# Kernel optimization log

Hardware: AMD Instinct MI355X
Metric: run time of the kernel (lower is better)

## Reference

```python
import jax, jax.numpy as jnp
import numpy as np

N_RAYS, MAX_S, N_VOX, EMB, HID, L_VIEW = 8192, 64, 100000, 32, 128, 4


def view_pe(d):
    # NeRF positional encoding of view dirs: [N,3] -> [N, 3 + 6*L_VIEW]
    freqs = 2.0 ** jnp.arange(L_VIEW, dtype=d.dtype)
    ang = (d[..., None] * freqs).reshape(*d.shape[:-1], -1)  # [N, 3*L]
    return jnp.concatenate([d, jnp.sin(ang), jnp.cos(ang)], -1)


def setup_inputs() -> dict:
    key = jax.random.key(0)
    ks = jax.random.split(key, 16)
    rays_d = jax.random.normal(ks[0], (N_RAYS, 3), dtype=jnp.float32)
    rays_d = rays_d / jnp.linalg.norm(rays_d, axis=-1, keepdims=True)
    pts = jax.random.uniform(ks[1], (N_RAYS, MAX_S, 3), dtype=jnp.float32)
    t_vals = jnp.sort(jax.random.uniform(ks[2], (N_RAYS, MAX_S), dtype=jnp.float32) * 4.0, axis=-1)
    dists = jnp.concatenate([t_vals[:, 1:] - t_vals[:, :-1], jnp.full((N_RAYS, 1), 0.05, jnp.float32)], -1)
    # ragged per-ray sample counts -> -1 padded p2v_idx (as produced by the voxel point sampler)
    counts = jax.random.randint(ks[3], (N_RAYS,), 1, MAX_S + 1)
    ray_hits = jax.random.bernoulli(ks[4], 0.9, (N_RAYS,))
    valid = (jnp.arange(MAX_S)[None, :] < counts[:, None]) & ray_hits[:, None]
    idx = jax.random.randint(ks[5], (N_RAYS, MAX_S), 0, N_VOX)
    p2v_idx = jnp.where(valid, idx, -1).astype(jnp.int32)

    def lin(k, i, o):
        return jax.random.normal(k, (i, o), dtype=jnp.float32) * np.float32(1.0 / np.sqrt(i))

    return dict(
        rays_d=rays_d, pts=pts, t_vals=t_vals, dists=dists,
        p2v_idx=p2v_idx, ray_hits=ray_hits,
        vox_emb=jax.random.normal(ks[6], (N_VOX, EMB), dtype=jnp.float32) * 0.1,
        Wpts=lin(ks[7], 3, EMB),
        W1=lin(ks[8], EMB, HID), b1=jnp.zeros((HID,), jnp.float32),
        W2=lin(ks[9], HID, HID), b2=jnp.zeros((HID,), jnp.float32),
        Wsig=lin(ks[10], HID, 1), bsig=jnp.zeros((1,), jnp.float32),
        Wfeat=lin(ks[11], HID, HID), bfeat=jnp.zeros((HID,), jnp.float32),
        Wc1=lin(ks[12], HID + 3 + 6 * L_VIEW, 64), bc1=jnp.zeros((64,), jnp.float32),
        Wc2=lin(ks[13], 64, 3), bc2=jnp.zeros((3,), jnp.float32),
    )


def reference(rays_d, pts, t_vals, dists, vox_emb, Wpts, W1, b1, W2, b2,
              Wsig, bsig, Wfeat, bfeat, Wc1, bc1, Wc2, bc2, p2v_idx, ray_hits):
    mask = p2v_idx >= 0                                   # [N,S] valid samples (mask_pts)
    idx = jnp.where(mask, p2v_idx, 0)
    # voxel_embedder: per-point voxel embedding gather + positional lift
    ve = vox_emb[idx] + pts @ Wpts                        # [N,S,EMB]
    h = jax.nn.relu(ve @ W1 + b1)
    h = jax.nn.relu(h @ W2 + b2)                          # [N,S,HID]
    sigma = (h @ Wsig + bsig)[..., 0]                     # [N,S]
    feat = h @ Wfeat + bfeat                              # [N,S,HID]
    vemb = view_pe(rays_d)                                # [N,27]
    vemb = jnp.broadcast_to(vemb[:, None, :], (feat.shape[0], feat.shape[1], vemb.shape[-1]))
    c = jax.nn.relu(jnp.concatenate([feat, vemb], -1) @ Wc1 + bc1)
    rgb_raw = c @ Wc2 + bc2                               # [N,S,3]
    # masked_scatter semantics: invalid slots are 0 before the min_color remap
    rgb = (jnp.where(mask[..., None], rgb_raw, 0.0) + 1.0) * 0.5   # min_color = -1
    free_energy = jnp.where(mask, jax.nn.relu(sigma) * dists, 0.0)  # [N,S]
    # volumetric_rendering(with_dist=True)
    shifted = jnp.concatenate([jnp.zeros_like(free_energy[:, :1]), free_energy[:, :-1]], -1)
    T = jnp.exp(-jnp.cumsum(shifted, -1))
    weights = (1.0 - jnp.exp(-free_energy)) * T           # [N,S]
    comp_rgb = jnp.einsum('ns,nsc->nc', weights, rgb)     # [N,3]
    acc = weights.sum(-1)                                 # [N]
    depth = (weights * t_vals).sum(-1)
    disp = 1.0 / jnp.maximum(1e-10, depth / jnp.maximum(acc, 1e-10))
    # fill_in for missed rays (white_bkgd=False -> fill with 0)
    comp_rgb = jnp.where(ray_hits[:, None], comp_rgb, 0.0)
    disp = jnp.where(ray_hits, disp, 0.0)
    acc = jnp.where(ray_hits, acc, 0.0)
    return comp_rgb, disp, acc
```

## Files before the change

### kernel.cpp

```cpp
#include <hip/hip_runtime.h>
#include <stdint.h>


#define NRAYS 8192
#define MAXS  64
#define EMB   32
#define HID   128
#define NPE   27
#define CH    64
#define NPTS  (NRAYS * MAXS)
#define RCAP  16384

#define WS_WCOMB  0
#define WS_WPE    (WS_WCOMB + HID*CH)
#define WS_BCOMB  (WS_WPE + 32*CH)
#define WS_CCINIT (WS_BCOMB + CH)
#define WS_COUNTS (WS_CCINIT + NRAYS*CH)
#define WS_OFFS   (WS_COUNTS + NRAYS)
#define WS_TOTAL  (WS_OFFS + NRAYS)
#define WS_RCNT   (WS_TOTAL + 1)
#define WS_LIST   (WS_TOTAL + 4)
#define WS_PTOUT  (WS_LIST + NPTS)
#define WS_FRAGS  (WS_PTOUT + 4*NPTS)
#define WS_RLIST  (WS_FRAGS + 56*2*64*4)
#define WS_PTSC   (WS_RLIST + RCAP)

typedef __attribute__((ext_vector_type(8))) short bf16x8;
typedef __attribute__((ext_vector_type(4))) float f32x4;
union FI { int i[4]; int4 v; bf16x8 f; };

#define MFMA16(a, b, c) __builtin_amdgcn_mfma_f32_16x16x32_bf16(a, b, c, 0, 0, 0)

__device__ __forceinline__ f32x4 mfma3(bf16x8 ah, bf16x8 al, bf16x8 bh, bf16x8 bl,
                                       f32x4 c) {
  c = MFMA16(al, bh, c);
  c = MFMA16(ah, bl, c);
  c = MFMA16(ah, bh, c);
  return c;
}

__device__ __forceinline__ void split8(const float* x, bf16x8& hi, bf16x8& lo) {
  FI H, L;
#pragma unroll
  for (int r = 0; r < 4; ++r) {
    unsigned u0 = __float_as_uint(x[2 * r]);
    unsigned u1 = __float_as_uint(x[2 * r + 1]);
    unsigned h0 = u0 & 0xffff0000u, h1 = u1 & 0xffff0000u;
    unsigned l0 = __float_as_uint(x[2 * r] - __uint_as_float(h0));
    unsigned l1 = __float_as_uint(x[2 * r + 1] - __uint_as_float(h1));
    H.i[r] = (int)((h0 >> 16) | (h1 & 0xffff0000u));
    L.i[r] = (int)((l0 >> 16) | (l1 & 0xffff0000u));
  }
  hi = H.f; lo = L.f;
}

__device__ __forceinline__ int packword(float v) {
  unsigned u = __float_as_uint(v);
  unsigned hb = u & 0xffff0000u;
  unsigned lb = __float_as_uint(v - __uint_as_float(hb));
  return (int)((u >> 16) | (lb & 0xffff0000u));
}

__device__ __forceinline__ void unpack8(const int* w, bf16x8& hi, bf16x8& lo) {
  FI H, L;
#pragma unroll
  for (int r = 0; r < 4; ++r) {
    unsigned w0 = (unsigned)w[2 * r], w1 = (unsigned)w[2 * r + 1];
    H.i[r] = (int)((w0 & 0xffffu) | (w1 << 16));
    L.i[r] = (int)((w0 >> 16) | (w1 & 0xffff0000u));
  }
  hi = H.f; lo = L.f;
}

__global__ __launch_bounds__(256) void prep_kernel(
    const float* __restrict__ Wfeat, const float* __restrict__ bfeat,
    const float* __restrict__ Wc1, const float* __restrict__ bc1,
    float* __restrict__ ws) {
  int idx = blockIdx.x * 256 + threadIdx.x;
  if (idx < HID * CH) {
    int m = idx >> 6, j = idx & 63;
    float s = 0.f;
    for (int f = 0; f < HID; ++f) s = fmaf(Wfeat[m * HID + f], Wc1[f * CH + j], s);
    ws[WS_WCOMB + idx] = s;
    return;
  }
  idx -= HID * CH;
  if (idx < 32 * CH) {
    int v = idx >> 6, j = idx & 63;
    ws[WS_WPE + idx] = (v < NPE) ? Wc1[(HID + v) * CH + j] : 0.f;
    return;
  }
  idx -= 32 * CH;
  if (idx < CH) {
    float s = bc1[idx];
    for (int f = 0; f < HID; ++f) s = fmaf(bfeat[f], Wc1[f * CH + idx], s);
    ws[WS_BCOMB + idx] = s;
    return;
  }
  idx -= CH;
  if (idx < 2) ((int*)(ws + WS_TOTAL))[idx] = 0;
}

__global__ __launch_bounds__(256) void prep2_kernel(
    const float* __restrict__ W1, const float* __restrict__ W2,
    float* __restrict__ ws) {
  int t = blockIdx.x * 256 + threadIdx.x;
  if (t >= 56 * 64) return;
  const int fid = t >> 6, lane = t & 63;
  const int n16 = lane & 15, quad = lane >> 4;
  float x[8];
  if (fid < 8) {
    const int n = fid * 16 + n16, k0 = quad * 8;
#pragma unroll
    for (int j = 0; j < 8; ++j) x[j] = W1[(k0 + j) * HID + n];
  } else if (fid < 40) {
    const int f = fid - 8, nt = f >> 2, s = f & 3;
    const int n = nt * 16 + n16, k0 = s * 32 + quad * 8;
#pragma unroll
    for (int j = 0; j < 8; ++j) x[j] = W2[(k0 + j) * HID + n];
  } else {
    const int f = fid - 40, nt = f >> 2, s = f & 3;
    const int n = nt * 16 + n16, k0 = s * 32 + quad * 8;
#pragma unroll
    for (int j = 0; j < 8; ++j) x[j] = ws[WS_WCOMB + (k0 + j) * CH + n];
  }
  FI H, L;
#pragma unroll
  for (int r = 0; r < 4; ++r) {
    unsigned u0 = __float_as_uint(x[2 * r]);
    unsigned u1 = __float_as_uint(x[2 * r + 1]);
    unsigned h0 = u0 & 0xffff0000u, h1 = u1 & 0xffff0000u;
    unsigned l0 = __float_as_uint(x[2 * r] - __uint_as_float(h0));
    unsigned l1 = __float_as_uint(x[2 * r + 1] - __uint_as_float(h1));
    H.i[r] = (int)((h0 >> 16) | (h1 & 0xffff0000u));
    L.i[r] = (int)((l0 >> 16) | (l1 & 0xffff0000u));
  }
  int4* o = (int4*)(ws + WS_FRAGS);
  o[(fid * 2 + 0) * 64 + lane] = H.v;
  o[(fid * 2 + 1) * 64 + lane] = L.v;
}

__global__ __launch_bounds__(256) void count_pe_kernel(
    const float* __restrict__ rays_d, const int* __restrict__ p2v,
    float* __restrict__ ws) {
  const int tid = threadIdx.x;
  const int ray = blockIdx.x * 4 + (tid >> 6);
  const int lane = tid & 63;
  const int v = p2v[ray * MAXS + lane];
  const unsigned long long ball = __ballot(v >= 0);
  if (lane == 0) ((int*)(ws + WS_COUNTS))[ray] = __popcll(ball);

  const float d0 = rays_d[ray * 3 + 0];
  const float d1 = rays_d[ray * 3 + 1];
  const float d2 = rays_d[ray * 3 + 2];
  float vemb[NPE];
  vemb[0] = d0; vemb[1] = d1; vemb[2] = d2;
#pragma unroll
  for (int i = 0; i < 3; ++i) {
    const float di = (i == 0) ? d0 : (i == 1) ? d1 : d2;
#pragma unroll
    for (int l = 0; l < 4; ++l) {
      const float ang = di * (float)(1 << l);
      vemb[3 + i * 4 + l] = __sinf(ang);
      vemb[3 + 12 + i * 4 + l] = __cosf(ang);
    }
  }
  float s = ws[WS_BCOMB + lane];
  const float* wpe = ws + WS_WPE;
#pragma unroll
  for (int vv = 0; vv < NPE; ++vv) s = fmaf(vemb[vv], wpe[vv * CH + lane], s);
  ws[WS_CCINIT + ray * CH + lane] = s;
}

__global__ __launch_bounds__(1024) void scan_kernel(float* __restrict__ ws) {
  const int* counts = (const int*)(ws + WS_COUNTS);
  int* offs = (int*)(ws + WS_OFFS);
  int* totalp = (int*)(ws + WS_TOTAL);
  __shared__ int wsum[16];
  const int tid = threadIdx.x;
  const int lane = tid & 63;
  const int base = tid * 8;
  if (tid == 0) ((int*)(ws + WS_RCNT))[0] = 0;
  int c[8], e[8];
  int run = 0;
#pragma unroll
  for (int i = 0; i < 8; ++i) { c[i] = counts[base + i]; e[i] = run; run += c[i]; }
  int inc = run;
#pragma unroll
  for (int off = 1; off < 64; off <<= 1) {
    int u = __shfl_up(inc, off, 64);
    if (lane >= off) inc += u;
  }
  const int wexcl = inc - run;
  if (lane == 63) wsum[tid >> 6] = inc;
  __syncthreads();
  if (tid < 16) {
    int v = wsum[tid];
    int inc2 = v;
#pragma unroll
    for (int off = 1; off < 16; off <<= 1) {
      int u = __shfl_up(inc2, off, 64);
      if (tid >= off) inc2 += u;
    }
    wsum[tid] = inc2 - v;
    if (tid == 15) totalp[0] = inc2;
  }
  __syncthreads();
  const int wbase = wsum[tid >> 6];
#pragma unroll
  for (int i = 0; i < 8; ++i) offs[base + i] = wbase + wexcl + e[i];
}

__global__ __launch_bounds__(256) void list_kernel(
    const int* __restrict__ p2v, const float* __restrict__ pts,
    float* __restrict__ ws) {
  const int tid = threadIdx.x;
  const int ray = blockIdx.x * 4 + (tid >> 6);
  const int lane = tid & 63;
  const int pidx = ray * MAXS + lane;
  const int gidx = p2v[pidx];
  const bool valid = gidx >= 0;
  const unsigned long long ball = __ballot(valid);
  const int rank = __popcll(ball & ((1ull << lane) - 1ull));
  if (valid) {
    const int off = ((const int*)(ws + WS_OFFS))[ray];
    const int slot = off + rank;
    ((int*)(ws + WS_LIST))[slot] = pidx;
    float4 pc;
    pc.x = pts[pidx * 3 + 0];
    pc.y = pts[pidx * 3 + 1];
    pc.z = pts[pidx * 3 + 2];
    pc.w = __int_as_float(gidx);
    ((float4*)(ws + WS_PTSC))[slot] = pc;
  }
}

__device__ __forceinline__ void ve_frag(const float* __restrict__ vox_emb,
                                        const float* __restrict__ Wpts,
                                        float4 pc, int quad,
                                        bf16x8& hi, bf16x8& lo) {
  float x[8];
  const int gidx = __float_as_int(pc.w);
  const float4* vr = (const float4*)vox_emb + gidx * 8 + quad * 2;
  const float4 va = vr[0], vb = vr[1];
  const float px = pc.x, py = pc.y, pz = pc.z;
  const float4* wp = (const float4*)Wpts;
  const float4 wa0 = wp[quad * 2 + 0], wa1 = wp[quad * 2 + 1];
  const float4 wb0 = wp[8 + quad * 2 + 0], wb1 = wp[8 + quad * 2 + 1];
  const float4 wc0 = wp[16 + quad * 2 + 0], wc1 = wp[16 + quad * 2 + 1];
  x[0] = va.x + fmaf(px, wa0.x, fmaf(py, wb0.x, pz * wc0.x));
  x[1] = va.y + fmaf(px, wa0.y, fmaf(py, wb0.y, pz * wc0.y));
  x[2] = va.z + fmaf(px, wa0.z, fmaf(py, wb0.z, pz * wc0.z));
  x[3] = va.w + fmaf(px, wa0.w, fmaf(py, wb0.w, pz * wc0.w));
  x[4] = vb.x + fmaf(px, wa1.x, fmaf(py, wb1.x, pz * wc1.x));
  x[5] = vb.y + fmaf(px, wa1.y, fmaf(py, wb1.y, pz * wc1.y));
  x[6] = vb.z + fmaf(px, wa1.z, fmaf(py, wb1.z, pz * wc1.z));
  x[7] = vb.w + fmaf(px, wa1.w, fmaf(py, wb1.w, pz * wc1.w));
  split8(x, hi, lo);
}

#define LSTRIDE 133

__global__ __launch_bounds__(128, 2) void mlp_mfma(
    const float* __restrict__ vox_emb, const float* __restrict__ Wpts,
    const float* __restrict__ b1, const float* __restrict__ b2,
    const float* __restrict__ Wsig, const float* __restrict__ bsig,
    const float* __restrict__ Wc2, const float* __restrict__ bc2,
    float* __restrict__ ws) {
  __shared__ int alds[64 * LSTRIDE];
  const int tid = threadIdx.x;
  const int wave = tid >> 6, lane = tid & 63;
  const int n16 = lane & 15, quad = lane >> 4;
  const int total = ((const int*)(ws + WS_TOTAL))[0];
  const int base = blockIdx.x * 64 + wave * 32;
  if (base >= total) return;
  const int* list = (const int*)(ws + WS_LIST);
  const int slot0 = min(base + n16, total - 1);
  const int slot1 = min(base + 16 + n16, total - 1);
  const int pidx0 = list[slot0];
  const int pidx1 = list[slot1];
  const float4 pc0 = ((const float4*)(ws + WS_PTSC))[slot0];
  const float4 pc1 = ((const float4*)(ws + WS_PTSC))[slot1];
  const int4* fb = (const int4*)(ws + WS_FRAGS);

  int4 B1f[16];
#pragma unroll
  for (int i = 0; i < 16; ++i) B1f[i] = fb[i * 64 + lane];

  bf16x8 a0h, a0l, a1h, a1l;
  ve_frag(vox_emb, Wpts, pc0, quad, a0h, a0l);
  ve_frag(vox_emb, Wpts, pc1, quad, a1h, a1l);

  int4 BL[2][16];
#pragma unroll
  for (int nt = 0; nt < 8; ++nt) {
    BL[0][2 * nt]     = fb[((8 + nt * 4) * 2 + 0) * 64 + lane];
    BL[0][2 * nt + 1] = fb[((8 + nt * 4) * 2 + 1) * 64 + lane];
  }

  f32x4 h[2][8];
#pragma unroll
  for (int nt = 0; nt < 8; ++nt) {
    const float bb = b1[nt * 16 + n16];
    h[0][nt] = (f32x4){bb, bb, bb, bb};
    h[1][nt] = h[0][nt];
  }
#pragma unroll
  for (int nt = 0; nt < 8; ++nt) {
    FI H, L; H.v = B1f[2 * nt]; L.v = B1f[2 * nt + 1];
    h[0][nt] = mfma3(a0h, a0l, H.f, L.f, h[0][nt]);
    h[1][nt] = mfma3(a1h, a1l, H.f, L.f, h[1][nt]);
  }
#pragma unroll
  for (int mt = 0; mt < 2; ++mt)
#pragma unroll
    for (int nt = 0; nt < 8; ++nt)
#pragma unroll
      for (int r = 0; r < 4; ++r) {
        const float v = fmaxf(h[mt][nt][r], 0.f);
        alds[(wave * 32 + mt * 16 + quad * 4 + r) * LSTRIDE + nt * 16 + n16] = packword(v);
      }

  f32x4 g[2][8];
#pragma unroll
  for (int nt = 0; nt < 8; ++nt) {
    const float bb = b2[nt * 16 + n16];
    g[0][nt] = (f32x4){bb, bb, bb, bb};
    g[1][nt] = g[0][nt];
  }
  const int rb0 = (wave * 32 + n16) * LSTRIDE;
  const int rb1 = rb0 + 16 * LSTRIDE;
#pragma unroll
  for (int s = 0; s < 4; ++s) {
    if (s < 3) {
#pragma unroll
      for (int nt = 0; nt < 8; ++nt) {
        BL[(s + 1) & 1][2 * nt]     = fb[((8 + nt * 4 + s + 1) * 2 + 0) * 64 + lane];
        BL[(s + 1) & 1][2 * nt + 1] = fb[((8 + nt * 4 + s + 1) * 2 + 1) * 64 + lane];
      }
    }
    int w0[8], w1[8];
#pragma unroll
    for (int j = 0; j < 8; ++j) {
      w0[j] = alds[rb0 + s * 32 + quad * 8 + j];
      w1[j] = alds[rb1 + s * 32 + quad * 8 + j];
    }
    bf16x8 A0h, A0l, A1h, A1l;
    unpack8(w0, A0h, A0l);
    unpack8(w1, A1h, A1l);
#pragma unroll
    for (int nt = 0; nt < 8; ++nt) {
      FI H, L; H.v = BL[s & 1][2 * nt]; L.v = BL[s & 1][2 * nt + 1];
      g[0][nt] = mfma3(A0h, A0l, H.f, L.f, g[0][nt]);
      g[1][nt] = mfma3(A1h, A1l, H.f, L.f, g[1][nt]);
    }
  }

  int pm[2][4];
#pragma unroll
  for (int mt = 0; mt < 2; ++mt)
#pragma unroll
    for (int r = 0; r < 4; ++r)
      pm[mt][r] = __shfl(mt ? pidx1 : pidx0, quad * 4 + r, 64);
  int4 BC[2][8];
#pragma unroll
  for (int nt = 0; nt < 4; ++nt) {
    BC[0][2 * nt]     = fb[((40 + nt * 4) * 2 + 0) * 64 + lane];
    BC[0][2 * nt + 1] = fb[((40 + nt * 4) * 2 + 1) * 64 + lane];
  }
  f32x4 cacc[2][4];
#pragma unroll
  for (int mt = 0; mt < 2; ++mt)
#pragma unroll
    for (int nt = 0; nt < 4; ++nt)
#pragma unroll
      for (int r = 0; r < 4; ++r)
        cacc[mt][nt][r] = ws[WS_CCINIT + (pm[mt][r] >> 6) * CH + nt * 16 + n16];

  float sg[2][4] = {{0.f, 0.f, 0.f, 0.f}, {0.f, 0.f, 0.f, 0.f}};
#pragma unroll
  for (int nt = 0; nt < 8; ++nt) {
    const float sv = Wsig[nt * 16 + n16];
#pragma unroll
    for (int mt = 0; mt < 2; ++mt)
#pragma unroll
      for (int r = 0; r < 4; ++r) {
        const float v = fmaxf(g[mt][nt][r], 0.f);
        sg[mt][r] = fmaf(v, sv, sg[mt][r]);
        alds[(wave * 32 + mt * 16 + quad * 4 + r) * LSTRIDE + nt * 16 + n16] = packword(v);
      }
  }
#pragma unroll
  for (int mask = 1; mask < 16; mask <<= 1)
#pragma unroll
    for (int mt = 0; mt < 2; ++mt)
#pragma unroll
      for (int r = 0; r < 4; ++r) sg[mt][r] += __shfl_xor(sg[mt][r], mask, 64);

#pragma unroll
  for (int s = 0; s < 4; ++s) {
    if (s < 3) {
#pragma unroll
      for (int nt = 0; nt < 4; ++nt) {
        BC[(s + 1) & 1][2 * nt]     = fb[((40 + nt * 4 + s + 1) * 2 + 0) * 64 + lane];
        BC[(s + 1) & 1][2 * nt + 1] = fb[((40 + nt * 4 + s + 1) * 2 + 1) * 64 + lane];
      }
    }
    int w0[8], w1[8];
#pragma unroll
    for (int j = 0; j < 8; ++j) {
      w0[j] = alds[rb0 + s * 32 + quad * 8 + j];
      w1[j] = alds[rb1 + s * 32 + quad * 8 + j];
    }
    bf16x8 A0h, A0l, A1h, A1l;
    unpack8(w0, A0h, A0l);
    unpack8(w1, A1h, A1l);
#pragma unroll
    for (int nt = 0; nt < 4; ++nt) {
      FI H, L; H.v = BC[s & 1][2 * nt]; L.v = BC[s & 1][2 * nt + 1];
      cacc[0][nt] = mfma3(A0h, A0l, H.f, L.f, cacc[0][nt]);
      cacc[1][nt] = mfma3(A1h, A1l, H.f, L.f, cacc[1][nt]);
    }
  }

  float cr[2][3][4];
#pragma unroll
  for (int mt = 0; mt < 2; ++mt)
#pragma unroll
    for (int c = 0; c < 3; ++c)
#pragma unroll
      for (int r = 0; r < 4; ++r) cr[mt][c][r] = 0.f;
#pragma unroll
  for (int nt = 0; nt < 4; ++nt) {
    const int j = nt * 16 + n16;
    const float w0 = Wc2[j * 3 + 0], w1c = Wc2[j * 3 + 1], w2c = Wc2[j * 3 + 2];
#pragma unroll
    for (int mt = 0; mt < 2; ++mt)
#pragma unroll
      for (int r = 0; r < 4; ++r) {
        const float cv = fmaxf(cacc[mt][nt][r], 0.f);
        cr[mt][0][r] = fmaf(cv, w0, cr[mt][0][r]);
        cr[mt][1][r] = fmaf(cv, w1c, cr[mt][1][r]);
        cr[mt][2][r] = fmaf(cv, w2c, cr[mt][2][r]);
      }
  }
#pragma unroll
  for (int mask = 1; mask < 16; mask <<= 1)
#pragma unroll
    for (int mt = 0; mt < 2; ++mt)
#pragma unroll
      for (int c = 0; c < 3; ++c)
#pragma unroll
        for (int r = 0; r < 4; ++r) cr[mt][c][r] += __shfl_xor(cr[mt][c][r], mask, 64);

  if (n16 == 0) {
    const float bs = bsig[0];
    const float bcr = bc2[0], bcg = bc2[1], bcb = bc2[2];
#pragma unroll
    for (int mt = 0; mt < 2; ++mt)
#pragma unroll
      for (int r = 0; r < 4; ++r) {
        const int m = mt * 16 + quad * 4 + r;
        if (base + m < total) {
          const int pid = pm[mt][r];
          const float sig = sg[mt][r] + bs;
          ((float4*)(ws + WS_PTOUT))[pid] =
              make_float4(sig, cr[mt][0][r] + bcr, cr[mt][1][r] + bcg, cr[mt][2][r] + bcb);
          if (fabsf(sig) < 0.006f) {
            const int ri = atomicAdd((int*)(ws + WS_RCNT), 1);
            if (ri < RCAP) ((int*)(ws + WS_RLIST))[ri] = pid;
          }
        }
      }
  }
}

__device__ __forceinline__ float wave_sum(float v) {
#pragma unroll
  for (int off = 32; off > 0; off >>= 1) v += __shfl_down(v, off, 64);
  return v;
}

__global__ __launch_bounds__(256) void repair_kernel(
    const float* __restrict__ pts, const int* __restrict__ p2v,
    const float* __restrict__ vox_emb, const float* __restrict__ Wpts,
    const float* __restrict__ W1, const float* __restrict__ b1,
    const float* __restrict__ W2, const float* __restrict__ b2,
    const float* __restrict__ Wsig, const float* __restrict__ bsig,
    float* __restrict__ ws) {
  __shared__ float h1s[4][HID];
  const int wv = threadIdx.x >> 6, lane = threadIdx.x & 63;
  const int cnt = min(((const int*)(ws + WS_RCNT))[0], RCAP);
  const int nw = gridDim.x * 4;
  for (int i = blockIdx.x * 4 + wv; i < cnt; i += nw) {
    const int pidx = ((const int*)(ws + WS_RLIST))[i];
    const int gidx = p2v[pidx];
    const float px = pts[pidx * 3 + 0];
    const float py = pts[pidx * 3 + 1];
    const float pz = pts[pidx * 3 + 2];
    float ve[EMB];
#pragma unroll
    for (int e = 0; e < EMB; ++e)
      ve[e] = vox_emb[gidx * EMB + e] +
              fmaf(px, Wpts[e], fmaf(py, Wpts[EMB + e], pz * Wpts[2 * EMB + e]));
    float s0 = b1[lane], s1 = b1[lane + 64];
#pragma unroll
    for (int k = 0; k < EMB; ++k) {
      const float x = ve[k];
      s0 = fmaf(x, W1[k * HID + lane], s0);
      s1 = fmaf(x, W1[k * HID + lane + 64], s1);
    }
    h1s[wv][lane] = fmaxf(s0, 0.f);
    h1s[wv][lane + 64] = fmaxf(s1, 0.f);
    float t0 = b2[lane], t1 = b2[lane + 64];
    for (int k = 0; k < HID; ++k) {
      const float x = h1s[wv][k];
      t0 = fmaf(x, W2[k * HID + lane], t0);
      t1 = fmaf(x, W2[k * HID + lane + 64], t1);
    }
    float sp = fmaf(fmaxf(t0, 0.f), Wsig[lane], fmaxf(t1, 0.f) * Wsig[lane + 64]);
    sp = wave_sum(sp);
    if (lane == 0) ws[WS_PTOUT + 4 * pidx + 0] = sp + bsig[0];
  }
}

__device__ __forceinline__ float wave_prefix_excl(float v, int lane) {
  float inc = v;
#pragma unroll
  for (int off = 1; off < 64; off <<= 1) {
    float u = __shfl_up(inc, off, 64);
    if (lane >= off) inc += u;
  }
  return inc - v;
}

__global__ __launch_bounds__(256) void render_kernel(
    const float* __restrict__ t_vals, const float* __restrict__ dists,
    const int* __restrict__ p2v, const float* __restrict__ ws,
    float* __restrict__ out_rgb, float* __restrict__ out_disp,
    float* __restrict__ out_acc) {
  const int tid = threadIdx.x;
  const int ray = blockIdx.x * 4 + (tid >> 6);
  const int lane = tid & 63;
  const int pidx = ray * MAXS + lane;

  const int vidx = p2v[pidx];
  const bool hit = (__shfl(vidx, 0, 64) >= 0);
  if (!hit) {
    if (lane < 3) out_rgb[ray * 3 + lane] = 0.f;
    if (lane == 0) { out_disp[ray] = 0.f; out_acc[ray] = 0.f; }
    return;
  }
  const bool valid = vidx >= 0;

  const float4 pv = ((const float4*)(ws + WS_PTOUT))[pidx];
  const float fe = valid ? fmaxf(pv.x, 0.f) * dists[pidx] : 0.f;
  const float pref = wave_prefix_excl(fe, lane);
  const float T = __expf(-pref);
  const float w = (1.f - __expf(-fe)) * T;
  const float tv = t_vals[pidx];

  const float crgb0 = wave_sum(w * (pv.y + 1.f) * 0.5f);
  const float crgb1 = wave_sum(w * (pv.z + 1.f) * 0.5f);
  const float crgb2 = wave_sum(w * (pv.w + 1.f) * 0.5f);
  const float accs = wave_sum(w);
  const float depth = wave_sum(w * tv);

  if (lane == 0) {
    out_rgb[ray * 3 + 0] = crgb0;
    out_rgb[ray * 3 + 1] = crgb1;
    out_rgb[ray * 3 + 2] = crgb2;
    const float disp = 1.f / fmaxf(1e-10f, depth / fmaxf(accs, 1e-10f));
    out_disp[ray] = disp;
    out_acc[ray] = accs;
  }
}

extern "C" void kernel_launch(void* const* d_in, const int* in_sizes, int n_in,
                              void* d_out, int out_size, void* d_ws, size_t ws_size,
                              hipStream_t stream) {
  const float* rays_d  = (const float*)d_in[0];
  const float* pts     = (const float*)d_in[1];
  const float* t_vals  = (const float*)d_in[2];
  const float* dists   = (const float*)d_in[3];
  const int*   p2v     = (const int*)d_in[4];
  const float* vox_emb = (const float*)d_in[6];
  const float* Wpts    = (const float*)d_in[7];
  const float* W1      = (const float*)d_in[8];
  const float* b1      = (const float*)d_in[9];
  const float* W2      = (const float*)d_in[10];
  const float* b2      = (const float*)d_in[11];
  const float* Wsig    = (const float*)d_in[12];
  const float* bsig    = (const float*)d_in[13];
  const float* Wfeat   = (const float*)d_in[14];
  const float* bfeat   = (const float*)d_in[15];
  const float* Wc1     = (const float*)d_in[16];
  const float* bc1     = (const float*)d_in[17];
  const float* Wc2     = (const float*)d_in[18];
  const float* bc2     = (const float*)d_in[19];

  float* ws = (float*)d_ws;
  float* out = (float*)d_out;
  float* out_rgb = out;
  float* out_disp = out + NRAYS * 3;
  float* out_acc = out + NRAYS * 4;

  hipLaunchKernelGGL(prep_kernel, dim3(41), dim3(256), 0, stream,
                     Wfeat, bfeat, Wc1, bc1, ws);
  hipLaunchKernelGGL(prep2_kernel, dim3(14), dim3(256), 0, stream, W1, W2, ws);
  hipLaunchKernelGGL(count_pe_kernel, dim3(NRAYS / 4), dim3(256), 0, stream,
                     rays_d, p2v, ws);
  hipLaunchKernelGGL(scan_kernel, dim3(1), dim3(1024), 0, stream, ws);
  hipLaunchKernelGGL(list_kernel, dim3(NRAYS / 4), dim3(256), 0, stream,
                     p2v, pts, ws);
  hipLaunchKernelGGL(mlp_mfma, dim3(NPTS / 64), dim3(128), 0, stream,
                     vox_emb, Wpts, b1, b2, Wsig, bsig, Wc2, bc2, ws);
  hipLaunchKernelGGL(repair_kernel, dim3(128), dim3(256), 0, stream,
                     pts, p2v, vox_emb, Wpts, W1, b1, W2, b2, Wsig, bsig, ws);
  hipLaunchKernelGGL(render_kernel, dim3(NRAYS / 4), dim3(256), 0, stream,
                     t_vals, dists, p2v, ws, out_rgb, out_disp, out_acc);
}
```

Baseline: 260.5 us.

## Fold weight prep and sigma repair into neighbouring kernels to cut launches

Merges the three prep kernels (combined-weight product, fragment packing, per-ray count/PE) into one launch. The Wfeat·Wc1 product is now computed inline during fragment packing, and the bias/PE projection is recomputed per ray from Wc1. Near-zero-sigma points are no longer recomputed by a separate repair kernel fed through an atomic list; instead, each wave in the render kernel ballots its low-|sigma| samples and recomputes them in FP32 in place. This removes three launches, the atomic counter and the repair list. The cost is redundant per-ray work (a 128-term bias dot product for every ray) and divergent repair loops inside render.

```diff
diff --git a/kernel.cpp b/kernel.cpp
--- a/kernel.cpp
+++ b/kernel.cpp
@@ -9,27 +9,22 @@
 #define NPE   27
 #define CH    64
 #define NPTS  (NRAYS * MAXS)
-#define RCAP  16384
-
-#define WS_WCOMB  0
-#define WS_WPE    (WS_WCOMB + HID*CH)
-#define WS_BCOMB  (WS_WPE + 32*CH)
-#define WS_CCINIT (WS_BCOMB + CH)
+
+#define WS_CCINIT 0
 #define WS_COUNTS (WS_CCINIT + NRAYS*CH)
 #define WS_OFFS   (WS_COUNTS + NRAYS)
 #define WS_TOTAL  (WS_OFFS + NRAYS)
-#define WS_RCNT   (WS_TOTAL + 1)
 #define WS_LIST   (WS_TOTAL + 4)
 #define WS_PTOUT  (WS_LIST + NPTS)
 #define WS_FRAGS  (WS_PTOUT + 4*NPTS)
-#define WS_RLIST  (WS_FRAGS + 56*2*64*4)
-#define WS_PTSC   (WS_RLIST + RCAP)
+#define WS_PTSC   (WS_FRAGS + 56*2*64*4)
 
 typedef __attribute__((ext_vector_type(8))) short bf16x8;
 typedef __attribute__((ext_vector_type(4))) float f32x4;
 union FI { int i[4]; int4 v; bf16x8 f; };
 
 #define MFMA16(a, b, c) __builtin_amdgcn_mfma_f32_16x16x32_bf16(a, b, c, 0, 0, 0)
+#define LSTRIDE 133
 
 __device__ __forceinline__ f32x4 mfma3(bf16x8 ah, bf16x8 al, bf16x8 bh, bf16x8 bl,
                                        f32x4 c) {
@@ -72,79 +67,72 @@
   hi = H.f; lo = L.f;
 }
 
-__global__ __launch_bounds__(256) void prep_kernel(
+__device__ __forceinline__ float wave_sum(float v) {
+#pragma unroll
+  for (int off = 32; off > 0; off >>= 1) v += __shfl_down(v, off, 64);
+  return v;
+}
+
+__device__ __forceinline__ float wave_prefix_excl(float v, int lane) {
+  float inc = v;
+#pragma unroll
+  for (int off = 1; off < 64; off <<= 1) {
+    float u = __shfl_up(inc, off, 64);
+    if (lane >= off) inc += u;
+  }
+  return inc - v;
+}
+
+__global__ __launch_bounds__(256) void prepA_kernel(
+    const float* __restrict__ W1, const float* __restrict__ W2,
     const float* __restrict__ Wfeat, const float* __restrict__ bfeat,
     const float* __restrict__ Wc1, const float* __restrict__ bc1,
-    float* __restrict__ ws) {
-  int idx = blockIdx.x * 256 + threadIdx.x;
-  if (idx < HID * CH) {
-    int m = idx >> 6, j = idx & 63;
-    float s = 0.f;
-    for (int f = 0; f < HID; ++f) s = fmaf(Wfeat[m * HID + f], Wc1[f * CH + j], s);
-    ws[WS_WCOMB + idx] = s;
-    return;
-  }
-  idx -= HID * CH;
-  if (idx < 32 * CH) {
-    int v = idx >> 6, j = idx & 63;
-    ws[WS_WPE + idx] = (v < NPE) ? Wc1[(HID + v) * CH + j] : 0.f;
-    return;
-  }
-  idx -= 32 * CH;
-  if (idx < CH) {
-    float s = bc1[idx];
-    for (int f = 0; f < HID; ++f) s = fmaf(bfeat[f], Wc1[f * CH + idx], s);
-    ws[WS_BCOMB + idx] = s;
-    return;
-  }
-  idx -= CH;
-  if (idx < 2) ((int*)(ws + WS_TOTAL))[idx] = 0;
-}
-
-__global__ __launch_bounds__(256) void prep2_kernel(
-    const float* __restrict__ W1, const float* __restrict__ W2,
-    float* __restrict__ ws) {
-  int t = blockIdx.x * 256 + threadIdx.x;
-  if (t >= 56 * 64) return;
-  const int fid = t >> 6, lane = t & 63;
-  const int n16 = lane & 15, quad = lane >> 4;
-  float x[8];
-  if (fid < 8) {
-    const int n = fid * 16 + n16, k0 = quad * 8;
-#pragma unroll
-    for (int j = 0; j < 8; ++j) x[j] = W1[(k0 + j) * HID + n];
-  } else if (fid < 40) {
-    const int f = fid - 8, nt = f >> 2, s = f & 3;
-    const int n = nt * 16 + n16, k0 = s * 32 + quad * 8;
-#pragma unroll
-    for (int j = 0; j < 8; ++j) x[j] = W2[(k0 + j) * HID + n];
-  } else {
-    const int f = fid - 40, nt = f >> 2, s = f & 3;
-    const int n = nt * 16 + n16, k0 = s * 32 + quad * 8;
-#pragma unroll
-    for (int j = 0; j < 8; ++j) x[j] = ws[WS_WCOMB + (k0 + j) * CH + n];
-  }
-  FI H, L;
-#pragma unroll
-  for (int r = 0; r < 4; ++r) {
-    unsigned u0 = __float_as_uint(x[2 * r]);
-    unsigned u1 = __float_as_uint(x[2 * r + 1]);
-    unsigned h0 = u0 & 0xffff0000u, h1 = u1 & 0xffff0000u;
-    unsigned l0 = __float_as_uint(x[2 * r] - __uint_as_float(h0));
-    unsigned l1 = __float_as_uint(x[2 * r + 1] - __uint_as_float(h1));
-    H.i[r] = (int)((h0 >> 16) | (h1 & 0xffff0000u));
-    L.i[r] = (int)((l0 >> 16) | (l1 & 0xffff0000u));
-  }
-  int4* o = (int4*)(ws + WS_FRAGS);
-  o[(fid * 2 + 0) * 64 + lane] = H.v;
-  o[(fid * 2 + 1) * 64 + lane] = L.v;
-}
-
-__global__ __launch_bounds__(256) void count_pe_kernel(
     const float* __restrict__ rays_d, const int* __restrict__ p2v,
     float* __restrict__ ws) {
   const int tid = threadIdx.x;
-  const int ray = blockIdx.x * 4 + (tid >> 6);
+  if (blockIdx.x < 14) {
+    const int idx = blockIdx.x * 256 + tid;
+    if (idx >= 56 * 64) return;
+    const int fid = idx >> 6, lane = idx & 63;
+    const int n16 = lane & 15, quad = lane >> 4;
+    float x[8];
+    if (fid < 8) {
+      const int n = fid * 16 + n16, k0 = quad * 8;
+#pragma unroll
+      for (int j = 0; j < 8; ++j) x[j] = W1[(k0 + j) * HID + n];
+    } else if (fid < 40) {
+      const int f = fid - 8, nt = f >> 2, s = f & 3;
+      const int n = nt * 16 + n16, k0 = s * 32 + quad * 8;
+#pragma unroll
+      for (int j = 0; j < 8; ++j) x[j] = W2[(k0 + j) * HID + n];
+    } else {
+      const int f = fid - 40, nt = f >> 2, s = f & 3;
+      const int n = nt * 16 + n16, k0 = s * 32 + quad * 8;
+#pragma unroll
+      for (int j = 0; j < 8; ++j) {
+        float sum = 0.f;
+        const float* wf = Wfeat + (k0 + j) * HID;
+        for (int ff = 0; ff < HID; ++ff) sum = fmaf(wf[ff], Wc1[ff * CH + n], sum);
+        x[j] = sum;
+      }
+    }
+    FI H, L;
+#pragma unroll
+    for (int r = 0; r < 4; ++r) {
+      unsigned u0 = __float_as_uint(x[2 * r]);
+      unsigned u1 = __float_as_uint(x[2 * r + 1]);
+      unsigned h0 = u0 & 0xffff0000u, h1 = u1 & 0xffff0000u;
+      unsigned l0 = __float_as_uint(x[2 * r] - __uint_as_float(h0));
+      unsigned l1 = __float_as_uint(x[2 * r + 1] - __uint_as_float(h1));
+      H.i[r] = (int)((h0 >> 16) | (h1 & 0xffff0000u));
+      L.i[r] = (int)((l0 >> 16) | (l1 & 0xffff0000u));
+    }
+    int4* o = (int4*)(ws + WS_FRAGS);
+    o[(fid * 2 + 0) * 64 + lane] = H.v;
+    o[(fid * 2 + 1) * 64 + lane] = L.v;
+    return;
+  }
+  const int ray = (blockIdx.x - 14) * 4 + (tid >> 6);
   const int lane = tid & 63;
   const int v = p2v[ray * MAXS + lane];
   const unsigned long long ball = __ballot(v >= 0);
@@ -165,10 +153,11 @@
       vemb[3 + 12 + i * 4 + l] = __cosf(ang);
     }
   }
-  float s = ws[WS_BCOMB + lane];
-  const float* wpe = ws + WS_WPE;
-#pragma unroll
-  for (int vv = 0; vv < NPE; ++vv) s = fmaf(vemb[vv], wpe[vv * CH + lane], s);
+  float s = bc1[lane];
+#pragma unroll 1
+  for (int f = 0; f < HID; ++f) s = fmaf(bfeat[f], Wc1[f * CH + lane], s);
+#pragma unroll
+  for (int vv = 0; vv < NPE; ++vv) s = fmaf(vemb[vv], Wc1[(HID + vv) * CH + lane], s);
   ws[WS_CCINIT + ray * CH + lane] = s;
 }
 
@@ -180,7 +169,6 @@
   const int tid = threadIdx.x;
   const int lane = tid & 63;
   const int base = tid * 8;
-  if (tid == 0) ((int*)(ws + WS_RCNT))[0] = 0;
   int c[8], e[8];
   int run = 0;
 #pragma unroll
@@ -259,8 +247,6 @@
   split8(x, hi, lo);
 }
 
-#define LSTRIDE 133
-
 __global__ __launch_bounds__(128, 2) void mlp_mfma(
     const float* __restrict__ vox_emb, const float* __restrict__ Wpts,
     const float* __restrict__ b1, const float* __restrict__ b2,
@@ -462,81 +448,22 @@
       for (int r = 0; r < 4; ++r) {
         const int m = mt * 16 + quad * 4 + r;
         if (base + m < total) {
-          const int pid = pm[mt][r];
-          const float sig = sg[mt][r] + bs;
-          ((float4*)(ws + WS_PTOUT))[pid] =
-              make_float4(sig, cr[mt][0][r] + bcr, cr[mt][1][r] + bcg, cr[mt][2][r] + bcb);
-          if (fabsf(sig) < 0.006f) {
-            const int ri = atomicAdd((int*)(ws + WS_RCNT), 1);
-            if (ri < RCAP) ((int*)(ws + WS_RLIST))[ri] = pid;
-          }
+          ((float4*)(ws + WS_PTOUT))[pm[mt][r]] =
+              make_float4(sg[mt][r] + bs, cr[mt][0][r] + bcr,
+                          cr[mt][1][r] + bcg, cr[mt][2][r] + bcb);
         }
       }
   }
 }
 
-__device__ __forceinline__ float wave_sum(float v) {
-#pragma unroll
-  for (int off = 32; off > 0; off >>= 1) v += __shfl_down(v, off, 64);
-  return v;
-}
-
-__global__ __launch_bounds__(256) void repair_kernel(
-    const float* __restrict__ pts, const int* __restrict__ p2v,
+__global__ __launch_bounds__(256) void render_kernel(
+    const float* __restrict__ t_vals, const float* __restrict__ dists,
+    const int* __restrict__ p2v, const float* __restrict__ pts,
     const float* __restrict__ vox_emb, const float* __restrict__ Wpts,
     const float* __restrict__ W1, const float* __restrict__ b1,
     const float* __restrict__ W2, const float* __restrict__ b2,
     const float* __restrict__ Wsig, const float* __restrict__ bsig,
-    float* __restrict__ ws) {
-  __shared__ float h1s[4][HID];
-  const int wv = threadIdx.x >> 6, lane = threadIdx.x & 63;
-  const int cnt = min(((const int*)(ws + WS_RCNT))[0], RCAP);
-  const int nw = gridDim.x * 4;
-  for (int i = blockIdx.x * 4 + wv; i < cnt; i += nw) {
-    const int pidx = ((const int*)(ws + WS_RLIST))[i];
-    const int gidx = p2v[pidx];
-    const float px = pts[pidx * 3 + 0];
-    const float py = pts[pidx * 3 + 1];
-    const float pz = pts[pidx * 3 + 2];
-    float ve[EMB];
-#pragma unroll
-    for (int e = 0; e < EMB; ++e)
-      ve[e] = vox_emb[gidx * EMB + e] +
-              fmaf(px, Wpts[e], fmaf(py, Wpts[EMB + e], pz * Wpts[2 * EMB + e]));
-    float s0 = b1[lane], s1 = b1[lane + 64];
-#pragma unroll
-    for (int k = 0; k < EMB; ++k) {
-      const float x = ve[k];
-      s0 = fmaf(x, W1[k * HID + lane], s0);
-      s1 = fmaf(x, W1[k * HID + lane + 64], s1);
-    }
-    h1s[wv][lane] = fmaxf(s0, 0.f);
-    h1s[wv][lane + 64] = fmaxf(s1, 0.f);
-    float t0 = b2[lane], t1 = b2[lane + 64];
-    for (int k = 0; k < HID; ++k) {
-      const float x = h1s[wv][k];
-      t0 = fmaf(x, W2[k * HID + lane], t0);
-      t1 = fmaf(x, W2[k * HID + lane + 64], t1);
-    }
-    float sp = fmaf(fmaxf(t0, 0.f), Wsig[lane], fmaxf(t1, 0.f) * Wsig[lane + 64]);
-    sp = wave_sum(sp);
-    if (lane == 0) ws[WS_PTOUT + 4 * pidx + 0] = sp + bsig[0];
-  }
-}
-
-__device__ __forceinline__ float wave_prefix_excl(float v, int lane) {
-  float inc = v;
-#pragma unroll
-  for (int off = 1; off < 64; off <<= 1) {
-    float u = __shfl_up(inc, off, 64);
-    if (lane >= off) inc += u;
-  }
-  return inc - v;
-}
-
-__global__ __launch_bounds__(256) void render_kernel(
-    const float* __restrict__ t_vals, const float* __restrict__ dists,
-    const int* __restrict__ p2v, const float* __restrict__ ws,
+    const float* __restrict__ ws,
     float* __restrict__ out_rgb, float* __restrict__ out_disp,
     float* __restrict__ out_acc) {
   const int tid = threadIdx.x;
@@ -554,7 +481,47 @@
   const bool valid = vidx >= 0;
 
   const float4 pv = ((const float4*)(ws + WS_PTOUT))[pidx];
-  const float fe = valid ? fmaxf(pv.x, 0.f) * dists[pidx] : 0.f;
+  float sigx = pv.x;
+
+  unsigned long long need = __ballot(valid && fabsf(sigx) < 0.006f);
+  while (need) {
+    const int fl = (int)(__ffsll((long long)need) - 1);
+    need &= need - 1;
+    const int rpidx = ray * MAXS + fl;
+    const int gidx = __shfl(vidx, fl, 64);
+    const float px = pts[rpidx * 3 + 0];
+    const float py = pts[rpidx * 3 + 1];
+    const float pz = pts[rpidx * 3 + 2];
+    float s0 = b1[lane], s1 = b1[lane + 64];
+#pragma unroll
+    for (int k = 0; k < EMB; ++k) {
+      const float vek = vox_emb[gidx * EMB + k] +
+                        fmaf(px, Wpts[k], fmaf(py, Wpts[EMB + k], pz * Wpts[2 * EMB + k]));
+      s0 = fmaf(vek, W1[k * HID + lane], s0);
+      s1 = fmaf(vek, W1[k * HID + lane + 64], s1);
+    }
+    s0 = fmaxf(s0, 0.f);
+    s1 = fmaxf(s1, 0.f);
+    float t0 = b2[lane], t1 = b2[lane + 64];
+#pragma unroll
+    for (int k = 0; k < 64; ++k) {
+      const float hk = __shfl(s0, k, 64);
+      t0 = fmaf(hk, W2[k * HID + lane], t0);
+      t1 = fmaf(hk, W2[k * HID + lane + 64], t1);
+    }
+#pragma unroll
+    for (int k = 0; k < 64; ++k) {
+      const float hk = __shfl(s1, k, 64);
+      t0 = fmaf(hk, W2[(64 + k) * HID + lane], t0);
+      t1 = fmaf(hk, W2[(64 + k) * HID + lane + 64], t1);
+    }
+    float sp = fmaf(fmaxf(t0, 0.f), Wsig[lane], fmaxf(t1, 0.f) * Wsig[lane + 64]);
+    sp = wave_sum(sp);
+    sp = __shfl(sp, 0, 64) + bsig[0];
+    if (lane == fl) sigx = sp;
+  }
+
+  const float fe = valid ? fmaxf(sigx, 0.f) * dists[pidx] : 0.f;
   const float pref = wave_prefix_excl(fe, lane);
   const float T = __expf(-pref);
   const float w = (1.f - __expf(-fe)) * T;
@@ -605,18 +572,15 @@
   float* out_disp = out + NRAYS * 3;
   float* out_acc = out + NRAYS * 4;
 
-  hipLaunchKernelGGL(prep_kernel, dim3(41), dim3(256), 0, stream,
-                     Wfeat, bfeat, Wc1, bc1, ws);
-  hipLaunchKernelGGL(prep2_kernel, dim3(14), dim3(256), 0, stream, W1, W2, ws);
-  hipLaunchKernelGGL(count_pe_kernel, dim3(NRAYS / 4), dim3(256), 0, stream,
-                     rays_d, p2v, ws);
+  hipLaunchKernelGGL(prepA_kernel, dim3(14 + NRAYS / 4), dim3(256), 0, stream,
+                     W1, W2, Wfeat, bfeat, Wc1, bc1, rays_d, p2v, ws);
   hipLaunchKernelGGL(scan_kernel, dim3(1), dim3(1024), 0, stream, ws);
   hipLaunchKernelGGL(list_kernel, dim3(NRAYS / 4), dim3(256), 0, stream,
                      p2v, pts, ws);
   hipLaunchKernelGGL(mlp_mfma, dim3(NPTS / 64), dim3(128), 0, stream,
                      vox_emb, Wpts, b1, b2, Wsig, bsig, Wc2, bc2, ws);
-  hipLaunchKernelGGL(repair_kernel, dim3(128), dim3(256), 0, stream,
-                     pts, p2v, vox_emb, Wpts, W1, b1, W2, b2, Wsig, bsig, ws);
   hipLaunchKernelGGL(render_kernel, dim3(NRAYS / 4), dim3(256), 0, stream,
-                     t_vals, dists, p2v, ws, out_rgb, out_disp, out_acc);
-}
+                     t_vals, dists, p2v, pts, vox_emb, Wpts,
+                     W1, b1, W2, b2, Wsig, bsig, ws,
+                     out_rgb, out_disp, out_acc);
+}
```

After: 357.2 us. +37.1%, slower.
